# Performance work log

Hardware: AMD Instinct MI355X
Metric: run time of the kernel (lower is better)

Reference implementation:

```python
import jax, jax.numpy as jnp
import numpy as np

D_MODEL = 1024
N_HEADS = 16
D_K = D_MODEL // N_HEADS
LN_EPS = 1e-5


def setup_inputs() -> dict:
    key = jax.random.key(0)
    ks = jax.random.split(key, 11)
    s = 1.0 / np.sqrt(D_MODEL)
    x = jax.random.normal(ks[0], (4, 2048, D_MODEL), dtype=jnp.float32)
    W_q = jax.random.uniform(ks[1], (D_MODEL, D_MODEL), jnp.float32, -s, s)
    b_q = jax.random.uniform(ks[2], (D_MODEL,), jnp.float32, -s, s)
    W_k = jax.random.uniform(ks[3], (D_MODEL, D_MODEL), jnp.float32, -s, s)
    b_k = jax.random.uniform(ks[4], (D_MODEL,), jnp.float32, -s, s)
    W_v = jax.random.uniform(ks[5], (D_MODEL, D_MODEL), jnp.float32, -s, s)
    b_v = jax.random.uniform(ks[6], (D_MODEL,), jnp.float32, -s, s)
    W_o = jax.random.uniform(ks[7], (D_MODEL, D_MODEL), jnp.float32, -s, s)
    b_o = jax.random.uniform(ks[8], (D_MODEL,), jnp.float32, -s, s)
    ln_gamma = jnp.ones((D_MODEL,), jnp.float32)
    ln_beta = jnp.zeros((D_MODEL,), jnp.float32)
    return {"x": x, "W_q": W_q, "b_q": b_q, "W_k": W_k, "b_k": b_k,
            "W_v": W_v, "b_v": b_v, "W_o": W_o, "b_o": b_o,
            "ln_gamma": ln_gamma, "ln_beta": ln_beta}


def reference(x, W_q, b_q, W_k, b_k, W_v, b_v, W_o, b_o, ln_gamma, ln_beta):
    B, S, D = x.shape
    # Linear projections (torch Linear: x @ W.T + b); split into heads.
    def proj(W, b):
        y = jnp.einsum('bsd,ed->bse', x, W) + b
        return y.reshape(B, S, N_HEADS, D_K).transpose(0, 2, 1, 3)  # [B,H,S,dk]
    Q = proj(W_q, b_q)
    K = proj(W_k, b_k)
    V = proj(W_v, b_v)
    scores = jnp.einsum('bhqd,bhkd->bhqk', Q, K) / np.sqrt(D_K)
    attn = jax.nn.softmax(scores, axis=-1)  # dropout is identity in eval
    context = jnp.einsum('bhqk,bhkd->bhqd', attn, V)
    context = context.transpose(0, 2, 1, 3).reshape(B, S, D)
    out = jnp.einsum('bsd,ed->bse', context, W_o) + b_o
    h = x + out  # residual
    mu = jnp.mean(h, axis=-1, keepdims=True)
    var = jnp.mean(jnp.square(h - mu), axis=-1, keepdims=True)
    return (h - mu) / jnp.sqrt(var + LN_EPS) * ln_gamma + ln_beta
```

## Files before the change

### kernel.cpp

```cpp
#include <hip/hip_runtime.h>
#include <hip/hip_bf16.h>
#include <stdint.h>

typedef __attribute__((ext_vector_type(4))) float f32x4;
typedef __attribute__((ext_vector_type(8))) short bf16x8;
typedef __attribute__((ext_vector_type(4))) short bf16x4;
typedef __attribute__((ext_vector_type(4))) short s16x4;

__device__ __forceinline__ float b2f(short s) {
    union { uint32_t u; float f; } v; v.u = ((uint32_t)(uint16_t)s) << 16; return v.f;
}
__device__ __forceinline__ short f2b(float f) {
    union { float f; uint32_t u; } v; v.f = f;
    uint32_t r = v.u + 0x7FFF + ((v.u >> 16) & 1);
    return (short)(r >> 16);
}
__device__ __forceinline__ f32x4 zero4() { f32x4 z = {0.f, 0.f, 0.f, 0.f}; return z; }

__device__ __forceinline__ void async16(const void* g, void* l) {
    __builtin_amdgcn_global_load_lds(
        (const __attribute__((address_space(1))) void*)g,
        (__attribute__((address_space(3))) void*)l, 16, 0, 0);
}
__device__ __forceinline__ uint32_t lds_addr(const void* p) {
    return (uint32_t)(uintptr_t)(const __attribute__((address_space(3))) void*)p;
}
__device__ __forceinline__ float exp2fast(float x) {
    float r; asm("v_exp_f32 %0, %1" : "=v"(r) : "v"(x)); return r;
}
__device__ __forceinline__ uint32_t cvtpk(float lo, float hi) {
    uint32_t r; asm("v_cvt_pk_bf16_f32 %0, %1, %2" : "=v"(r) : "v"(lo), "v"(hi)); return r;
}

__global__ __launch_bounds__(256)
void cvt5(const float* __restrict__ x,
          const float* __restrict__ wq, const float* __restrict__ wk,
          const float* __restrict__ wv, const float* __restrict__ wo,
          short* __restrict__ xb, short* __restrict__ wqb, short* __restrict__ wkb,
          short* __restrict__ wvb, short* __restrict__ wob)
{
    const int b = blockIdx.x;
    const float* src; short* dst; size_t off;
    if (b < 8192) { src = x; dst = xb; off = (size_t)b * 1024; }
    else {
        const int wsel = (b - 8192) >> 10;
        off = (size_t)((b - 8192) & 1023) * 1024;
        switch (wsel) {
            case 0: src = wq; dst = wqb; break;
            case 1: src = wk; dst = wkb; break;
            case 2: src = wv; dst = wvb; break;
            default: src = wo; dst = wob; break;
        }
    }
    const int t = threadIdx.x;
    const float4 v = *(const float4*)(src + off + t * 4);
    s16x4 o;
    o[0] = f2b(v.x); o[1] = f2b(v.y); o[2] = f2b(v.z); o[3] = f2b(v.w);
    *(s16x4*)(dst + off + t * 4) = o;
}

template <bool OUTF32, bool RESID>
__device__ __forceinline__
void gemm_core(const short* __restrict__ Ab, const short* __restrict__ Bb,
               const float* __restrict__ bias, const float* __restrict__ resid,
               void* __restrict__ Cv, int m0, int n0col, int K, int N,
               short* lsA, short* lsB)
{
    const int t = threadIdx.x;
    const int wave = t >> 6, lane = t & 63;
    const int wr = wave >> 1, wc = wave & 1;
    const int lr = lane & 15, kg = lane >> 4;

    f32x4 acc[4][4];
#pragma unroll
    for (int m = 0; m < 4; ++m)
#pragma unroll
        for (int n = 0; n < 4; ++n) acc[m][n] = zero4();

    const int rG = t >> 3;
    const int cG = (((t & 7) ^ (rG & 7))) * 8;

    for (int k0 = 0; k0 < K; k0 += 64) {
        __syncthreads();
#pragma unroll
        for (int i = 0; i < 4; ++i) {
            async16(Ab + (size_t)(rG + 32 * i) * K + k0 + cG, &lsA[t * 8 + 2048 * i]);
            async16(Bb + (size_t)(rG + 32 * i) * K + k0 + cG, &lsB[t * 8 + 2048 * i]);
        }
        __syncthreads();

#pragma unroll
        for (int ks = 0; ks < 2; ++ks) {
            const int xc = ((ks * 4 + kg) ^ (lr & 7)) * 8;
            bf16x8 aF[4], bF[4];
#pragma unroll
            for (int m = 0; m < 4; ++m)
                aF[m] = *(const bf16x8*)&lsA[(wr * 64 + m * 16 + lr) * 64 + xc];
#pragma unroll
            for (int n = 0; n < 4; ++n)
                bF[n] = *(const bf16x8*)&lsB[(wc * 64 + n * 16 + lr) * 64 + xc];
#pragma unroll
            for (int m = 0; m < 4; ++m)
#pragma unroll
                for (int n = 0; n < 4; ++n)
                    acc[m][n] = __builtin_amdgcn_mfma_f32_16x16x32_bf16(aF[m], bF[n], acc[m][n], 0, 0, 0);
        }
    }

#pragma unroll
    for (int n = 0; n < 4; ++n) {
        const int col = n0col + wc * 64 + n * 16 + lr;
        const float bvv = bias[col];
#pragma unroll
        for (int m = 0; m < 4; ++m) {
            const int rowb = m0 + wr * 64 + m * 16 + kg * 4;
#pragma unroll
            for (int r = 0; r < 4; ++r) {
                const size_t idx = (size_t)(rowb + r) * N + col;
                float v = acc[m][n][r] + bvv;
                if (RESID) v += resid[idx];
                if (OUTF32) ((float*)Cv)[idx] = v;
                else        ((short*)Cv)[idx] = f2b(v);
            }
        }
    }
}

__global__ __launch_bounds__(256)
void gemm_qkv(const short* __restrict__ A, const short* __restrict__ Wcat,
              const float* __restrict__ bq, const float* __restrict__ bk,
              const float* __restrict__ bv,
              short* __restrict__ Qw, short* __restrict__ Kw, short* __restrict__ Vw)
{
    __shared__ short lsA[128 * 64];
    __shared__ short lsB[128 * 64];
    const int L = blockIdx.x;
    const int wgid = (L & 7) * 192 + (L >> 3);
    const int nb = wgid % 24;
    const int my = wgid / 24;
    const int tb = nb >> 3;
    const float* bias = (tb == 0) ? bq : (tb == 1) ? bk : bv;
    short* dst = (tb == 0) ? Qw : (tb == 1) ? Kw : Vw;
    gemm_core<false, false>(A + (size_t)my * 128 * 1024,
                            Wcat + (size_t)nb * 128 * 1024,
                            bias - (nb & 7) * 128,
                            nullptr, dst, my * 128, (nb & 7) * 128, 1024, 1024,
                            lsA, lsB);
}

__global__ __launch_bounds__(256)
void gemm_out(const short* __restrict__ A, const short* __restrict__ Bw,
              const float* __restrict__ bias, const float* __restrict__ resid,
              float* __restrict__ C)
{
    __shared__ short lsA[128 * 64];
    __shared__ short lsB[128 * 64];
    const int L = blockIdx.x;
    const int wgid = (L & 7) * 64 + (L >> 3);
    const int nb = wgid & 7, my = wgid >> 3;
    gemm_core<true, true>(A + (size_t)my * 128 * 1024,
                          Bw + (size_t)nb * 128 * 1024,
                          bias, resid, C, my * 128, nb * 128, 1024, 1024,
                          lsA, lsB);
}

__global__ __launch_bounds__(512)
void attn_fwd(const short* __restrict__ Q, const short* __restrict__ K,
              const short* __restrict__ V, short* __restrict__ ctx)
{
    __shared__ short lsK[2][64 * 64];
    __shared__ short lsV[2][64 * 64];
    __shared__ short lsP[8][16 * 64];

    const float C1 = 0.18033688011112042f;

    const int t = threadIdx.x, w = t >> 6, lane = t & 63;
    const int lr = lane & 15, kg = lane >> 4;
    const int bh = blockIdx.x;
    const size_t base = (size_t)(bh >> 4) * 2048 * 1024 + (size_t)(bh & 15) * 64;
    const short* Qg = Q + base;
    short* Og = ctx + base;
    const int q0 = blockIdx.y * 256 + w * 32;

    bf16x8 qB[2][2];
#pragma unroll
    for (int m = 0; m < 2; ++m)
#pragma unroll
        for (int ks = 0; ks < 2; ++ks)
            qB[m][ks] = *(const bf16x8*)(Qg + (size_t)(q0 + m * 16 + lr) * 1024 + ks * 32 + kg * 8);

    bf16x8 onesB;
#pragma unroll
    for (int j = 0; j < 8; ++j) onesB[j] = (short)0x3F80;

    const int rK  = t >> 3;
    const int cK  = (((t & 7) ^ (rK & 7))) * 8;
    const int kvV = (t & 127) >> 1;
    const int dV  = ((t >> 7) << 4) + (t & 1) * 8;
    const short* pK = K + base + (size_t)rK * 1024 + cK;
    const short* pV = V + base + (size_t)kvV * 1024 + dV;

    f32x4 o[2][4];
    f32x4 osum[2];
#pragma unroll
    for (int m = 0; m < 2; ++m) {
#pragma unroll
        for (int n = 0; n < 4; ++n) o[m][n] = zero4();
        osum[m] = zero4();
    }
    float mx[2] = {-1e30f, -1e30f};

    const int pmask = (lr & 7) << 3;
    short* lsPw = lsP[w];

    async16(pK, &lsK[0][t * 8]);
    async16(pV, &lsV[0][t * 8]);

    int buf = 0;
    for (int it = 0; it < 32; ++it) {
        __syncthreads();
        if (it + 1 < 32) {
            pK += 65536; pV += 65536;
            async16(pK, &lsK[buf ^ 1][t * 8]);
            async16(pV, &lsV[buf ^ 1][t * 8]);
        }
        const short* cbK = lsK[buf];
        const short* cbV = lsV[buf];

        f32x4 s[2][4];
        const int x0 = ((kg)     ^ (lr & 7)) * 8;
        const int x1 = ((4 + kg) ^ (lr & 7)) * 8;
        __builtin_amdgcn_s_setprio(1);
#pragma unroll
        for (int cb = 0; cb < 4; ++cb) {
            const bf16x8 kA0 = *(const bf16x8*)&cbK[(cb * 16 + lr) * 64 + x0];
            const bf16x8 kA1 = *(const bf16x8*)&cbK[(cb * 16 + lr) * 64 + x1];
#pragma unroll
            for (int m = 0; m < 2; ++m) {
                f32x4 a = __builtin_amdgcn_mfma_f32_16x16x32_bf16(kA0, qB[m][0], zero4(), 0, 0, 0);
                s[m][cb] = __builtin_amdgcn_mfma_f32_16x16x32_bf16(kA1, qB[m][1], a, 0, 0, 0);
            }
        }
        __builtin_amdgcn_s_setprio(0);

        float smax[2];
#pragma unroll
        for (int m = 0; m < 2; ++m) {
            float a = fmaxf(fmaxf(s[m][0][0], s[m][0][1]), fmaxf(s[m][0][2], s[m][0][3]));
            float b = fmaxf(fmaxf(s[m][1][0], s[m][1][1]), fmaxf(s[m][1][2], s[m][1][3]));
            float c = fmaxf(fmaxf(s[m][2][0], s[m][2][1]), fmaxf(s[m][2][2], s[m][2][3]));
            float d = fmaxf(fmaxf(s[m][3][0], s[m][3][1]), fmaxf(s[m][3][2], s[m][3][3]));
            float e = fmaxf(fmaxf(a, b), fmaxf(c, d));
            e = fmaxf(e, __shfl_xor(e, 16));
            e = fmaxf(e, __shfl_xor(e, 32));
            smax[m] = e;
        }

        if (!__all((smax[0] <= mx[0] + 64.f) && (smax[1] <= mx[1] + 64.f))) {
            float corrS[2];
#pragma unroll
            for (int m = 0; m < 2; ++m) {
                const float mnew = fmaxf(mx[m], smax[m]);
                corrS[m] = exp2fast((mx[m] - mnew) * C1);
                mx[m] = mnew;
            }
#pragma unroll
            for (int m = 0; m < 2; ++m) {
                f32x4 c;
#pragma unroll
                for (int r = 0; r < 4; ++r) c[r] = __shfl(corrS[m], kg * 4 + r);
#pragma unroll
                for (int n = 0; n < 4; ++n) {
                    o[m][n][0] *= c[0]; o[m][n][1] *= c[1];
                    o[m][n][2] *= c[2]; o[m][n][3] *= c[3];
                }
                osum[m][0] *= c[0]; osum[m][1] *= c[1];
                osum[m][2] *= c[2]; osum[m][3] *= c[3];
            }
        }

        bf16x4 tv[4][4];
#pragma unroll
        for (int n = 0; n < 4; ++n) {
            const uint32_t a = lds_addr(&cbV[n * 1024 + kg * 128 + lr]);
            asm volatile(
                "ds_read_b64_tr_b16 %0, %4\n\t"
                "ds_read_b64_tr_b16 %1, %4 offset:128\n\t"
                "ds_read_b64_tr_b16 %2, %4 offset:1024\n\t"
                "ds_read_b64_tr_b16 %3, %4 offset:1152"
                : "=&v"(tv[n][0]), "=&v"(tv[n][1]), "=&v"(tv[n][2]), "=&v"(tv[n][3])
                : "v"(a));
        }
        asm volatile("s_waitcnt lgkmcnt(0)" ::: "memory");
        __builtin_amdgcn_sched_barrier(0);

#pragma unroll
        for (int m = 0; m < 2; ++m) {
            const float nm2 = mx[m] * C1;
#pragma unroll
            for (int cb = 0; cb < 4; ++cb) {
                const float p0 = exp2fast(fmaf(s[m][cb][0], C1, -nm2));
                const float p1 = exp2fast(fmaf(s[m][cb][1], C1, -nm2));
                const float p2 = exp2fast(fmaf(s[m][cb][2], C1, -nm2));
                const float p3 = exp2fast(fmaf(s[m][cb][3], C1, -nm2));
                const int c0i = (cb * 16 + kg * 4) ^ pmask;
                *(uint32_t*)&lsPw[lr * 64 + c0i]     = cvtpk(p0, p1);
                *(uint32_t*)&lsPw[lr * 64 + c0i + 2] = cvtpk(p2, p3);
            }

            bf16x8 pA[2];
#pragma unroll
            for (int kh = 0; kh < 2; ++kh)
                pA[kh] = *(const bf16x8*)&lsPw[lr * 64 + ((kh * 32 + kg * 8) ^ pmask)];

            __builtin_amdgcn_s_setprio(1);
#pragma unroll
            for (int n = 0; n < 4; ++n) {
#pragma unroll
                for (int kh = 0; kh < 2; ++kh) {
                    const bf16x8 vB = __builtin_shufflevector(tv[n][kh * 2], tv[n][kh * 2 + 1],
                                                              0, 1, 2, 3, 4, 5, 6, 7);
                    o[m][n] = __builtin_amdgcn_mfma_f32_16x16x32_bf16(pA[kh], vB, o[m][n], 0, 0, 0);
                }
            }
            osum[m] = __builtin_amdgcn_mfma_f32_16x16x32_bf16(pA[0], onesB, osum[m], 0, 0, 0);
            osum[m] = __builtin_amdgcn_mfma_f32_16x16x32_bf16(pA[1], onesB, osum[m], 0, 0, 0);
            __builtin_amdgcn_s_setprio(0);
        }
        buf ^= 1;
    }

#pragma unroll
    for (int m = 0; m < 2; ++m) {
        f32x4 inv;
#pragma unroll
        for (int r = 0; r < 4; ++r) inv[r] = 1.0f / osum[m][r];
#pragma unroll
        for (int n = 0; n < 4; ++n)
#pragma unroll
            for (int r = 0; r < 4; ++r) {
                const int row = q0 + m * 16 + kg * 4 + r;
                Og[(size_t)row * 1024 + n * 16 + lr] = f2b(o[m][n][r] * inv[r]);
            }
    }
}

__global__ __launch_bounds__(256)
void ln_inplace(float* __restrict__ io, const float* __restrict__ gamma,
                const float* __restrict__ beta)
{
    __shared__ float redS[4];
    __shared__ float redQ[4];
    const int t = threadIdx.x, wave = t >> 6, lane = t & 63;
    const size_t rb = (size_t)blockIdx.x * 1024;

    float4 v4 = *(const float4*)&io[rb + t * 4];
    float v[4] = {v4.x, v4.y, v4.z, v4.w};

    float s = 0.f, sq = 0.f;
#pragma unroll
    for (int j = 0; j < 4; ++j) { s += v[j]; sq += v[j] * v[j]; }
#pragma unroll
    for (int off = 32; off; off >>= 1) {
        s  += __shfl_xor(s, off);
        sq += __shfl_xor(sq, off);
    }
    if (lane == 0) { redS[wave] = s; redQ[wave] = sq; }
    __syncthreads();
    const float mean = (redS[0] + redS[1] + redS[2] + redS[3]) * (1.0f / 1024.0f);
    const float ex2  = (redQ[0] + redQ[1] + redQ[2] + redQ[3]) * (1.0f / 1024.0f);
    const float var  = fmaxf(ex2 - mean * mean, 0.f);
    const float inv  = rsqrtf(var + 1e-5f);

    float4 o4;
    o4.x = (v[0] - mean) * inv * gamma[t * 4 + 0] + beta[t * 4 + 0];
    o4.y = (v[1] - mean) * inv * gamma[t * 4 + 1] + beta[t * 4 + 1];
    o4.z = (v[2] - mean) * inv * gamma[t * 4 + 2] + beta[t * 4 + 2];
    o4.w = (v[3] - mean) * inv * gamma[t * 4 + 3] + beta[t * 4 + 3];
    *(float4*)&io[rb + t * 4] = o4;
}

extern "C" void kernel_launch(void* const* d_in, const int* in_sizes, int n_in,
                              void* d_out, int out_size, void* d_ws, size_t ws_size,
                              hipStream_t stream)
{
    const float* x  = (const float*)d_in[0];
    const float* Wq = (const float*)d_in[1];
    const float* bq = (const float*)d_in[2];
    const float* Wk = (const float*)d_in[3];
    const float* bk = (const float*)d_in[4];
    const float* Wv = (const float*)d_in[5];
    const float* bv = (const float*)d_in[6];
    const float* Wo = (const float*)d_in[7];
    const float* bo = (const float*)d_in[8];
    const float* gamma = (const float*)d_in[9];
    const float* beta  = (const float*)d_in[10];

    const size_t NX = (size_t)8192 * 1024;
    const size_t NW = (size_t)1024 * 1024;

    short* xb  = (short*)d_ws;
    short* Wqb = xb + NX;
    short* Wkb = Wqb + NW;
    short* Wvb = Wkb + NW;
    short* Wob = Wvb + NW;
    short* Qw  = Wob + NW;
    short* Kw  = Qw + NX;
    short* Vw  = Kw + NX;
    short* Cw  = Vw + NX;
    float* out = (float*)d_out;

    cvt5<<<dim3(12288), dim3(256), 0, stream>>>(x, Wq, Wk, Wv, Wo, xb, Wqb, Wkb, Wvb, Wob);
    gemm_qkv<<<dim3(1536), dim3(256), 0, stream>>>(xb, Wqb, bq, bk, bv, Qw, Kw, Vw);
    attn_fwd<<<dim3(64, 8), dim3(512), 0, stream>>>(Qw, Kw, Vw, Cw);
    gemm_out<<<dim3(512), dim3(256), 0, stream>>>(Cw, Wob, bo, x, out);
    ln_inplace<<<dim3(8192), dim3(256), 0, stream>>>(out, gamma, beta);
}
```

Baseline: 239.4 us.

## Double-buffer GEMM LDS tiles with async prefetch and a K-step of 32

Restructures the shared GEMM core to double-buffer LDS. The next 32-wide K slice is loaded asynchronously while MFMAs run on the current one, with one barrier per iteration instead of two. This is meant to overlap global-load latency with compute. The tile K depth is halved and the XOR swizzle is removed, so LDS bank conflicts and per-iteration overhead may increase.

```diff
diff --git a/kernel.cpp b/kernel.cpp
--- a/kernel.cpp
+++ b/kernel.cpp
@@ -77,34 +77,44 @@
 #pragma unroll
         for (int n = 0; n < 4; ++n) acc[m][n] = zero4();
 
-    const int rG = t >> 3;
-    const int cG = (((t & 7) ^ (rG & 7))) * 8;
-
-    for (int k0 = 0; k0 < K; k0 += 64) {
+    const int r0 = t >> 2;
+    const int c0 = (t & 3) * 8;
+
+    async16(Ab + (size_t)r0 * K + c0,        &lsA[t * 8]);
+    async16(Ab + (size_t)(r0 + 64) * K + c0, &lsA[t * 8 + 2048]);
+    async16(Bb + (size_t)r0 * K + c0,        &lsB[t * 8]);
+    async16(Bb + (size_t)(r0 + 64) * K + c0, &lsB[t * 8 + 2048]);
+    __syncthreads();
+
+    int buf = 0;
+    for (int k0 = 0; k0 < K; k0 += 32) {
+        if (k0 + 32 < K) {
+            const int kn = k0 + 32;
+            short* dA = lsA + (buf ^ 1) * 4096;
+            short* dB = lsB + (buf ^ 1) * 4096;
+            async16(Ab + (size_t)r0 * K + kn + c0,        dA + t * 8);
+            async16(Ab + (size_t)(r0 + 64) * K + kn + c0, dA + t * 8 + 2048);
+            async16(Bb + (size_t)r0 * K + kn + c0,        dB + t * 8);
+            async16(Bb + (size_t)(r0 + 64) * K + kn + c0, dB + t * 8 + 2048);
+        }
+
+        const short* cA = lsA + buf * 4096;
+        const short* cB = lsB + buf * 4096;
+        bf16x8 aF[4], bF[4];
+#pragma unroll
+        for (int m = 0; m < 4; ++m)
+            aF[m] = *(const bf16x8*)&cA[(wr * 64 + m * 16 + lr) * 32 + kg * 8];
+#pragma unroll
+        for (int n = 0; n < 4; ++n)
+            bF[n] = *(const bf16x8*)&cB[(wc * 64 + n * 16 + lr) * 32 + kg * 8];
+#pragma unroll
+        for (int m = 0; m < 4; ++m)
+#pragma unroll
+            for (int n = 0; n < 4; ++n)
+                acc[m][n] = __builtin_amdgcn_mfma_f32_16x16x32_bf16(aF[m], bF[n], acc[m][n], 0, 0, 0);
+
         __syncthreads();
-#pragma unroll
-        for (int i = 0; i < 4; ++i) {
-            async16(Ab + (size_t)(rG + 32 * i) * K + k0 + cG, &lsA[t * 8 + 2048 * i]);
-            async16(Bb + (size_t)(rG + 32 * i) * K + k0 + cG, &lsB[t * 8 + 2048 * i]);
-        }
-        __syncthreads();
-
-#pragma unroll
-        for (int ks = 0; ks < 2; ++ks) {
-            const int xc = ((ks * 4 + kg) ^ (lr & 7)) * 8;
-            bf16x8 aF[4], bF[4];
-#pragma unroll
-            for (int m = 0; m < 4; ++m)
-                aF[m] = *(const bf16x8*)&lsA[(wr * 64 + m * 16 + lr) * 64 + xc];
-#pragma unroll
-            for (int n = 0; n < 4; ++n)
-                bF[n] = *(const bf16x8*)&lsB[(wc * 64 + n * 16 + lr) * 64 + xc];
-#pragma unroll
-            for (int m = 0; m < 4; ++m)
-#pragma unroll
-                for (int n = 0; n < 4; ++n)
-                    acc[m][n] = __builtin_amdgcn_mfma_f32_16x16x32_bf16(aF[m], bF[n], acc[m][n], 0, 0, 0);
-        }
+        buf ^= 1;
     }
 
 #pragma unroll
@@ -132,8 +142,8 @@
               const float* __restrict__ bv,
               short* __restrict__ Qw, short* __restrict__ Kw, short* __restrict__ Vw)
 {
-    __shared__ short lsA[128 * 64];
-    __shared__ short lsB[128 * 64];
+    __shared__ short lsA[2 * 128 * 32];
+    __shared__ short lsB[2 * 128 * 32];
     const int L = blockIdx.x;
     const int wgid = (L & 7) * 192 + (L >> 3);
     const int nb = wgid % 24;
@@ -153,8 +163,8 @@
               const float* __restrict__ bias, const float* __restrict__ resid,
               float* __restrict__ C)
 {
-    __shared__ short lsA[128 * 64];
-    __shared__ short lsB[128 * 64];
+    __shared__ short lsA[2 * 128 * 32];
+    __shared__ short lsB[2 * 128 * 32];
     const int L = blockIdx.x;
     const int wgid = (L & 7) * 64 + (L >> 3);
     const int nb = wgid & 7, my = wgid >> 3;
```

Result: no change. 242.0 us (+1.1%).
